# Kernel optimization log

Hardware: AMD Instinct MI355X
Metric: run time of the kernel (lower is better)

The kernel has to match this reference:

```python
import jax, jax.numpy as jnp
import numpy as np

# Multi-level feature-map spatial shapes (compile-time constants, as in Deformable DETR
# for an 800x1333 input with strides 8/16/32/64).
SPATIAL_SHAPES = ((100, 167), (50, 84), (25, 42), (13, 21))
NUM_KEYS = sum(h * w for h, w in SPATIAL_SHAPES)  # 22223


def setup_inputs() -> dict:
    key = jax.random.key(0)
    k1, k2, k3 = jax.random.split(key, 3)
    bs, nq, nh, d, nl, npt = 8, 900, 8, 32, 4, 4
    value = jax.random.normal(k1, (bs, NUM_KEYS, nh, d), jnp.float32)
    sampling_locations = jax.random.uniform(k2, (bs, nq, nh, nl, npt, 2), jnp.float32)
    aw = jax.random.uniform(k3, (bs, nq, nh, nl, npt), jnp.float32)
    # module applies softmax over (levels*points) before calling the kernel
    aw = jax.nn.softmax(aw.reshape(bs, nq, nh, nl * npt), axis=-1).reshape(bs, nq, nh, nl, npt)
    return {"value": value, "sampling_locations": sampling_locations, "attention_weights": aw}


def _bilinear_sample(v_flat, H, W, x, y):
    # v_flat: (bs, nh, H*W, d); x, y: (bs, nh, P) pixel coords (align_corners=False convention)
    x0 = jnp.floor(x)
    y0 = jnp.floor(y)
    x1 = x0 + 1.0
    y1 = y0 + 1.0
    wx1 = x - x0
    wx0 = 1.0 - wx1
    wy1 = y - y0
    wy0 = 1.0 - wy1

    def gather(xi, yi):
        # zero padding: out-of-bounds corners contribute 0 (grid_sample padding_mode='zeros')
        valid = (xi >= 0) & (xi <= W - 1) & (yi >= 0) & (yi <= H - 1)
        xc = jnp.clip(xi, 0, W - 1).astype(jnp.int32)
        yc = jnp.clip(yi, 0, H - 1).astype(jnp.int32)
        idx = yc * W + xc  # (bs, nh, P)
        s = jnp.take_along_axis(v_flat, idx[..., None], axis=2)  # (bs, nh, P, d)
        return jnp.where(valid[..., None], s, jnp.zeros((), v_flat.dtype))

    return (gather(x0, y0) * (wx0 * wy0)[..., None]
            + gather(x1, y0) * (wx1 * wy0)[..., None]
            + gather(x0, y1) * (wx0 * wy1)[..., None]
            + gather(x1, y1) * (wx1 * wy1)[..., None])


def reference(value, sampling_locations, attention_weights):
    # value: (bs, num_keys, nh, d)
    # sampling_locations: (bs, nq, nh, nl, npt, 2), normalized (x, y) in [0, 1]
    # attention_weights: (bs, nq, nh, nl, npt)
    bs, _, nh, d = value.shape
    _, nq, _, nl, npt, _ = sampling_locations.shape
    out = jnp.zeros((bs, nh, nq, d), value.dtype)
    start = 0
    for lvl, (H, W) in enumerate(SPATIAL_SHAPES):
        v = value[:, start:start + H * W]                     # (bs, H*W, nh, d)
        start += H * W
        v = jnp.transpose(v, (0, 2, 1, 3))                    # (bs, nh, H*W, d)
        loc = sampling_locations[:, :, :, lvl]                # (bs, nq, nh, npt, 2)
        # grid = 2*loc - 1; pixel coord (align_corners=False): (g+1)*S/2 - 0.5 = loc*S - 0.5
        x = loc[..., 0] * W - 0.5
        y = loc[..., 1] * H - 0.5
        x = jnp.transpose(x, (0, 2, 1, 3)).reshape(bs, nh, nq * npt)
        y = jnp.transpose(y, (0, 2, 1, 3)).reshape(bs, nh, nq * npt)
        sampled = _bilinear_sample(v, H, W, x, y).reshape(bs, nh, nq, npt, d)
        w = jnp.transpose(attention_weights[:, :, :, lvl], (0, 2, 1, 3))  # (bs, nh, nq, npt)
        out = out + jnp.einsum('bhqpd,bhqp->bhqd', sampled, w)
    # torch output is (bs, nq, nh*d) with head-major channel layout
    return jnp.transpose(out, (0, 2, 1, 3)).reshape(bs, nq, nh * d)
```

## Files before the change

kernel.cpp:

```cpp
#include <hip/hip_runtime.h>


#define BS 8
#define NQ 900
#define NH 8
#define NL 4
#define NPT 4
#define NUM_KEYS 22223

__global__ __launch_bounds__(256) void msda_kernel(
    const float* __restrict__ value,
    const float* __restrict__ loc,
    const float* __restrict__ aw,
    float* __restrict__ out)
{
    const int tid = blockIdx.x * 256 + threadIdx.x;
    const int cg  = tid & 7;
    const int lvl = (tid >> 3) & 3;
    const int h   = (tid >> 5) & 7;
    const int bq  = tid >> 8;
    const int b   = bq / NQ;

    const bool l01 = lvl < 2;
    const int H  = l01 ? (lvl == 0 ? 100 : 50)    : (lvl == 2 ? 25 : 13);
    const int W  = l01 ? (lvl == 0 ? 167 : 84)    : (lvl == 2 ? 42 : 21);
    const int St = l01 ? (lvl == 0 ? 0 : 16700)   : (lvl == 2 ? 20900 : 21950);

    const float4* __restrict__ v4 = (const float4*)value;
    const unsigned vbase = (unsigned)b * (NUM_KEYS * NH * 8) + h * 8 + cg
                         + (unsigned)St * (NH * 8);
    const unsigned rowstride = (unsigned)W * (NH * 8);

    const int lidx = (bq * NH + h) * NL + lvl;
    const float4* __restrict__ loc4 = (const float4*)loc;
    const float4* __restrict__ aw4  = (const float4*)aw;
    const float4 xy01 = loc4[lidx * 2];
    const float4 xy23 = loc4[lidx * 2 + 1];
    const float4 wv   = aw4[lidx];

    const float xs[NPT] = {xy01.x, xy01.z, xy23.x, xy23.z};
    const float ys[NPT] = {xy01.y, xy01.w, xy23.y, xy23.w};
    const float ws[NPT] = {wv.x, wv.y, wv.z, wv.w};

    float4 acc = {0.f, 0.f, 0.f, 0.f};

    #pragma unroll
    for (int p = 0; p < NPT; ++p) {
        const float x = xs[p] * (float)W - 0.5f;
        const float y = ys[p] * (float)H - 0.5f;
        const float w = ws[p];
        const float fx0 = floorf(x);
        const float fy0 = floorf(y);
        const int x0 = (int)fx0;
        const int y0 = (int)fy0;
        float wx1 = x - fx0, wy1 = y - fy0;
        float wx0 = 1.f - wx1, wy0 = 1.f - wy1;

        wx0 = (x0 >= 0 && x0 <= W - 1)         ? wx0 : 0.f;
        wx1 = (x0 + 1 >= 0 && x0 + 1 <= W - 1) ? wx1 : 0.f;
        wy0 = (y0 >= 0 && y0 <= H - 1)         ? wy0 : 0.f;
        wy1 = (y0 + 1 >= 0 && y0 + 1 <= H - 1) ? wy1 : 0.f;

        const int x0c = min(max(x0, 0), W - 1);
        const int x1c = min(max(x0 + 1, 0), W - 1);
        const int y0c = min(max(y0, 0), H - 1);
        const int y1c = min(max(y0 + 1, 0), H - 1);

        const unsigned r0 = vbase + (unsigned)y0c * rowstride;
        const unsigned r1 = vbase + (unsigned)y1c * rowstride;

        const float4 v00 = v4[r0 + (unsigned)x0c * (NH * 8)];
        const float4 v01 = v4[r0 + (unsigned)x1c * (NH * 8)];
        const float4 v10 = v4[r1 + (unsigned)x0c * (NH * 8)];
        const float4 v11 = v4[r1 + (unsigned)x1c * (NH * 8)];

        const float s00 = w * wx0 * wy0;
        const float s01 = w * wx1 * wy0;
        const float s10 = w * wx0 * wy1;
        const float s11 = w * wx1 * wy1;

        acc.x = fmaf(s00, v00.x, acc.x); acc.y = fmaf(s00, v00.y, acc.y);
        acc.z = fmaf(s00, v00.z, acc.z); acc.w = fmaf(s00, v00.w, acc.w);
        acc.x = fmaf(s01, v01.x, acc.x); acc.y = fmaf(s01, v01.y, acc.y);
        acc.z = fmaf(s01, v01.z, acc.z); acc.w = fmaf(s01, v01.w, acc.w);
        acc.x = fmaf(s10, v10.x, acc.x); acc.y = fmaf(s10, v10.y, acc.y);
        acc.z = fmaf(s10, v10.z, acc.z); acc.w = fmaf(s10, v10.w, acc.w);
        acc.x = fmaf(s11, v11.x, acc.x); acc.y = fmaf(s11, v11.y, acc.y);
        acc.z = fmaf(s11, v11.z, acc.z); acc.w = fmaf(s11, v11.w, acc.w);
    }

    acc.x += __shfl_xor(acc.x, 8);  acc.y += __shfl_xor(acc.y, 8);
    acc.z += __shfl_xor(acc.z, 8);  acc.w += __shfl_xor(acc.w, 8);
    acc.x += __shfl_xor(acc.x, 16); acc.y += __shfl_xor(acc.y, 16);
    acc.z += __shfl_xor(acc.z, 16); acc.w += __shfl_xor(acc.w, 16);

    if (lvl == 0) {
        float4* __restrict__ out4 = (float4*)out;
        out4[(bq * NH + h) * 8 + cg] = acc;
    }
}

extern "C" void kernel_launch(void* const* d_in, const int* in_sizes, int n_in,
                              void* d_out, int out_size, void* d_ws, size_t ws_size,
                              hipStream_t stream) {
    const float* value = (const float*)d_in[0];
    const float* loc   = (const float*)d_in[1];
    const float* aw    = (const float*)d_in[2];
    float* outp = (float*)d_out;

    const int total = BS * NQ * NH * NL * 8;
    const int block = 256;
    const int grid = total / block;
    msda_kernel<<<grid, block, 0, stream>>>(value, loc, aw, outp);
}
```

Measured before the change: 254.2 us.

## Remap blocks so each block handles one head across eight queries

Thread blocks are reassigned so that each block covers a single head and batch for a chunk of eight queries, where before a block covered all heads of one query. Consecutive blocks cycle over heads, so the blocks resident at the same time read the same head slice of the value tensor. The aim is better L2 and cache locality for the gathered value rows. The cost is a ragged last chunk, since 113 chunks of eight is 904 rows, handled by an early return, plus a more scattered access pattern for the location and weight loads and the output stores.

```diff
diff --git a/kernel.cpp b/kernel.cpp
--- a/kernel.cpp
+++ b/kernel.cpp
@@ -7,6 +7,7 @@
 #define NL 4
 #define NPT 4
 #define NUM_KEYS 22223
+#define QCHUNKS 113
 
 __global__ __launch_bounds__(256) void msda_kernel(
     const float* __restrict__ value,
@@ -14,24 +15,29 @@
     const float* __restrict__ aw,
     float* __restrict__ out)
 {
-    const int tid = blockIdx.x * 256 + threadIdx.x;
-    const int cg  = tid & 7;
-    const int lvl = (tid >> 3) & 3;
-    const int h   = (tid >> 5) & 7;
-    const int bq  = tid >> 8;
-    const int b   = bq / NQ;
+    const int x  = blockIdx.x & 7;
+    const int t  = blockIdx.x >> 3;
+    const int b  = t / QCHUNKS;
+    const int qc = t - b * QCHUNKS;
+    const int h  = x;
+
+    const int cg  = threadIdx.x & 7;
+    const int lvl = (threadIdx.x >> 3) & 3;
+    const int qs  = threadIdx.x >> 5;
+    const int q   = qc * 8 + qs;
+    if (q >= NQ) return;
 
     const bool l01 = lvl < 2;
-    const int H  = l01 ? (lvl == 0 ? 100 : 50)    : (lvl == 2 ? 25 : 13);
-    const int W  = l01 ? (lvl == 0 ? 167 : 84)    : (lvl == 2 ? 42 : 21);
-    const int St = l01 ? (lvl == 0 ? 0 : 16700)   : (lvl == 2 ? 20900 : 21950);
+    const int H  = l01 ? (lvl == 0 ? 100 : 50)  : (lvl == 2 ? 25 : 13);
+    const int W  = l01 ? (lvl == 0 ? 167 : 84)  : (lvl == 2 ? 42 : 21);
+    const int St = l01 ? (lvl == 0 ? 0 : 16700) : (lvl == 2 ? 20900 : 21950);
 
     const float4* __restrict__ v4 = (const float4*)value;
     const unsigned vbase = (unsigned)b * (NUM_KEYS * NH * 8) + h * 8 + cg
                          + (unsigned)St * (NH * 8);
     const unsigned rowstride = (unsigned)W * (NH * 8);
 
-    const int lidx = (bq * NH + h) * NL + lvl;
+    const int lidx = ((b * NQ + q) * NH + h) * NL + lvl;
     const float4* __restrict__ loc4 = (const float4*)loc;
     const float4* __restrict__ aw4  = (const float4*)aw;
     const float4 xy01 = loc4[lidx * 2];
@@ -46,14 +52,14 @@
 
     #pragma unroll
     for (int p = 0; p < NPT; ++p) {
-        const float x = xs[p] * (float)W - 0.5f;
-        const float y = ys[p] * (float)H - 0.5f;
-        const float w = ws[p];
-        const float fx0 = floorf(x);
-        const float fy0 = floorf(y);
+        const float xf = xs[p] * (float)W - 0.5f;
+        const float yf = ys[p] * (float)H - 0.5f;
+        const float w  = ws[p];
+        const float fx0 = floorf(xf);
+        const float fy0 = floorf(yf);
         const int x0 = (int)fx0;
         const int y0 = (int)fy0;
-        float wx1 = x - fx0, wy1 = y - fy0;
+        float wx1 = xf - fx0, wy1 = yf - fy0;
         float wx0 = 1.f - wx1, wy0 = 1.f - wy1;
 
         wx0 = (x0 >= 0 && x0 <= W - 1)         ? wx0 : 0.f;
@@ -96,7 +102,7 @@
 
     if (lvl == 0) {
         float4* __restrict__ out4 = (float4*)out;
-        out4[(bq * NH + h) * 8 + cg] = acc;
+        out4[((b * NQ + q) * NH + h) * 8 + cg] = acc;
     }
 }
 
@@ -108,8 +114,6 @@
     const float* aw    = (const float*)d_in[2];
     float* outp = (float*)d_out;
 
-    const int total = BS * NQ * NH * NL * 8;
-    const int block = 256;
-    const int grid = total / block;
-    msda_kernel<<<grid, block, 0, stream>>>(value, loc, aw, outp);
+    const int grid = 8 * BS * QCHUNKS;
+    msda_kernel<<<grid, 256, 0, stream>>>(value, loc, aw, outp);
 }
```

After: 271.5 us. 6.8% more time.
